# Kernel tuning notes

Hardware: AMD Instinct MI355X
Metric: run time of the kernel (lower is better)

Reference implementation:

```python
import jax, jax.numpy as jnp
import numpy as np

EPS = 1e-5
NEG = -10000.0


def rel_shift(x):
    # x: [B, H, T1, T2] with T2 = 2*T1 - 1 -> returns [B, H, T1, T1]
    B, H, T1, T2 = x.shape
    x = jnp.pad(x, ((0, 0), (0, 0), (0, 0), (1, 0)))        # [B,H,T1,T2+1]
    x = x.reshape(B, H, T2 + 1, T1)[:, :, 1:, :].reshape(B, H, T1, T2)
    return x[:, :, :, : T2 // 2 + 1]


def setup_inputs() -> dict:
    key = jax.random.key(0)
    B, C, T, H = 4, 512, 1024, 8
    ks = jax.random.split(key, 16)
    s = 0.02
    inp = {
        "x": jax.random.normal(ks[0], (B, C, T), jnp.float32),
        "pos_emb": jax.random.normal(ks[1], (1, C, 2 * T - 1), jnp.float32),
        "x_mask": jnp.ones((B, 1, T), jnp.float32),
        "gamma": jnp.ones((C,), jnp.float32),
        "beta": jnp.zeros((C,), jnp.float32),
        "Wq": jax.random.normal(ks[2], (C, C), jnp.float32) * s,
        "bq": jnp.zeros((C,), jnp.float32),
        "Wk": jax.random.normal(ks[3], (C, C), jnp.float32) * s,
        "bk": jnp.zeros((C,), jnp.float32),
        "Wv": jax.random.normal(ks[4], (C, C), jnp.float32) * s,
        "bv": jnp.zeros((C,), jnp.float32),
        "Wp": jax.random.normal(ks[5], (C, C), jnp.float32) * s,
        "u_bias": jax.random.normal(ks[6], (H, C // H), jnp.float32) * s,
        "v_bias": jax.random.normal(ks[7], (H, C // H), jnp.float32) * s,
        "Wo": jax.random.normal(ks[8], (C, C), jnp.float32) * s,
        "bo": jnp.zeros((C,), jnp.float32),
    }
    return inp


def reference(x, pos_emb, x_mask, gamma, beta, Wq, bq, Wk, bk, Wv, bv, Wp,
              u_bias, v_bias, Wo, bo):
    B, C, T = x.shape
    H, Dh = u_bias.shape

    # channel LayerNorm (axis=1)
    mean = jnp.mean(x, axis=1, keepdims=True)
    var = jnp.mean((x - mean) ** 2, axis=1, keepdims=True)
    xn = (x - mean) * jax.lax.rsqrt(var + EPS)
    xn = xn * gamma[None, :, None] + beta[None, :, None]

    conv1x1 = lambda W, b, z: jnp.einsum('oc,bct->bot', W, z) + b[None, :, None]
    q = conv1x1(Wq, bq, xn).reshape(B, H, Dh, T)
    k = conv1x1(Wk, bk, xn).reshape(B, H, Dh, T)
    v = conv1x1(Wv, bv, xn).reshape(B, H, Dh, T)
    p = jnp.einsum('oc,xct->xot', Wp, pos_emb)          # [1, C, 2T-1], no bias
    p = p.reshape(p.shape[0], H, Dh, -1)[0]             # [H, Dh, 2T-1]

    content = jnp.einsum('bhdt,bhds->bhts', q + u_bias[None, :, :, None], k)
    pos = jnp.einsum('bhdt,hds->bhts', q + v_bias[None, :, :, None], p)
    pos = rel_shift(pos)                                 # [B, H, T, T]

    score = (content + pos) / jnp.sqrt(jnp.float32(C))
    attn_mask = x_mask[:, :, None, :] * x_mask[:, :, :, None]  # [B,1,T,T]
    score = jnp.where(attn_mask == 0, NEG, score)
    attn = jax.nn.softmax(score, axis=-1)

    # context[d,t] = sum_s v[d,s] * attn[s,t]
    ctx = jnp.einsum('bhds,bhst->bhdt', v, attn).reshape(B, C, T)
    return jnp.einsum('oc,bct->bot', Wo, ctx) + bo[None, :, None]
```

## Files before the change

kernel.cpp:

```cpp
#include <hip/hip_runtime.h>
#include <hip/hip_bf16.h>

typedef unsigned short u16;
typedef __bf16 bf16_t;
typedef bf16_t bf16x8 __attribute__((ext_vector_type(8)));
typedef float f32x4 __attribute__((ext_vector_type(4)));
typedef u16 u16x8 __attribute__((ext_vector_type(8)));

#define MFMA16(A,B,C) __builtin_amdgcn_mfma_f32_16x16x32_bf16(A,B,C,0,0,0)

#define CB 512
#define TT 1024
#define NH 8
#define DH 64
static __constant__ float kScale = 0.044194173824159216f;

static __device__ __forceinline__ u16 f2b(float f) {
  unsigned u = __float_as_uint(f);
  unsigned r = u + 0x7FFFu + ((u >> 16) & 1u);
  return (u16)(r >> 16);
}
static __device__ __forceinline__ float b2f(u16 u) {
  return __uint_as_float(((unsigned)u) << 16);
}
static __device__ __forceinline__ bf16x8 ldb8(const u16* p) {
  return *reinterpret_cast<const bf16x8*>(p);
}

__global__ __launch_bounds__(256)
void convert5(const float* __restrict__ Wq, const float* __restrict__ Wk,
              const float* __restrict__ Wv, const float* __restrict__ Wp,
              const float* __restrict__ Wo,
              u16* __restrict__ Wstk, u16* __restrict__ WoB)
{
  int i = blockIdx.x * 256 + threadIdx.x;
  int sel = i >> 15, loc = i & 32767;
  const float* src = (sel == 0) ? Wq : (sel == 1) ? Wk : (sel == 2) ? Wv
                   : (sel == 3) ? Wp : Wo;
  const float4 a = ((const float4*)src)[loc * 2 + 0];
  const float4 b = ((const float4*)src)[loc * 2 + 1];
  u16x8 o;
  o[0] = f2b(a.x); o[1] = f2b(a.y); o[2] = f2b(a.z); o[3] = f2b(a.w);
  o[4] = f2b(b.x); o[5] = f2b(b.y); o[6] = f2b(b.z); o[7] = f2b(b.w);
  u16* dst = (sel < 4) ? (Wstk + (size_t)i * 8) : (WoB + (size_t)loc * 8);
  *(u16x8*)dst = o;
}

__global__ __launch_bounds__(256)
void transpose_pe(const float* __restrict__ pe, u16* __restrict__ posT)
{
  __shared__ float tile[64][65];
  int j0 = blockIdx.x * 64, c0 = blockIdx.y * 64;
  for (int e = threadIdx.x; e < 4096; e += 256) {
    int cc = e >> 6, jj = e & 63;
    int j = j0 + jj;
    tile[jj][cc] = (j < 2047) ? pe[(size_t)(c0 + cc) * 2047 + j] : 0.f;
  }
  __syncthreads();
  for (int e = threadIdx.x; e < 4096; e += 256) {
    int jj = e >> 6, cc = e & 63;
    posT[(size_t)(j0 + jj) * 512 + c0 + cc] = f2b(tile[jj][cc]);
  }
}

__global__ __launch_bounds__(256)
void ln_kernel(const float* __restrict__ x, const float* __restrict__ gamma,
               const float* __restrict__ beta, u16* __restrict__ xnT)
{
  __shared__ float sred[8][33], ssred[8][33];
  int tl = threadIdx.x & 31, cg = threadIdx.x >> 5;
  int t = blockIdx.x * 32 + tl;
  int b = blockIdx.y;
  const float* xb = x + (size_t)b * CB * TT + t;
  float s = 0.f, ss = 0.f;
  for (int c = cg * 64; c < cg * 64 + 64; ++c) {
    float v = xb[(size_t)c * TT];
    s += v; ss += v * v;
  }
  sred[cg][tl] = s; ssred[cg][tl] = ss;
  __syncthreads();
  float S = 0.f, SS = 0.f;
  #pragma unroll
  for (int g = 0; g < 8; ++g) { S += sred[g][tl]; SS += ssred[g][tl]; }
  float mean = S * (1.f / 512.f);
  float var = SS * (1.f / 512.f) - mean * mean;
  float rstd = rsqrtf(var + 1e-5f);
  u16* orow = xnT + ((size_t)b * TT + t) * CB;
  for (int c8 = 0; c8 < 8; ++c8) {
    int c = cg * 64 + c8 * 8;
    u16x8 o;
    #pragma unroll
    for (int j = 0; j < 8; ++j) {
      float v = xb[(size_t)(c + j) * TT];
      o[j] = f2b((v - mean) * rstd * gamma[c + j] + beta[c + j]);
    }
    *(u16x8*)(orow + c) = o;
  }
}

template<int K, int OMODE>
__global__ __launch_bounds__(256)
void gemm2(const u16* __restrict__ A, const u16* __restrict__ XT,
           long xStride, long oStride, int Nout,
           const float* __restrict__ b0, void* __restrict__ outv)
{
  const int tid = threadIdx.x, w = tid >> 6, lane = tid & 63;
  const int ln16 = lane & 15, kg = lane >> 4;
  const int wm = w & 1, wn = w >> 1;
  const int m0 = blockIdx.y * 64 + wm * 32;
  const int n0 = blockIdx.x * 128 + wn * 64;
  const int z = blockIdx.z;
  const u16* Ar = A + (size_t)(m0 + ln16) * K + kg * 8;
  const u16* Br = XT + (size_t)z * xStride + (size_t)(n0 + ln16) * K + kg * 8;
  f32x4 acc[2][4] = {};
  #pragma unroll 2
  for (int ks = 0; ks < K / 32; ++ks) {
    bf16x8 a[2], bb[4];
    #pragma unroll
    for (int mt = 0; mt < 2; ++mt) a[mt] = ldb8(Ar + (size_t)mt * 16 * K + ks * 32);
    #pragma unroll
    for (int nt = 0; nt < 4; ++nt) bb[nt] = ldb8(Br + (size_t)nt * 16 * K + ks * 32);
    #pragma unroll
    for (int mt = 0; mt < 2; ++mt)
      #pragma unroll
      for (int nt = 0; nt < 4; ++nt)
        acc[mt][nt] = MFMA16(a[mt], bb[nt], acc[mt][nt]);
  }
  float add[2][4];
  #pragma unroll
  for (int mt = 0; mt < 2; ++mt)
    #pragma unroll
    for (int jr = 0; jr < 4; ++jr)
      add[mt][jr] = b0 ? b0[m0 + mt * 16 + kg * 4 + jr] : 0.f;
  #pragma unroll
  for (int mt = 0; mt < 2; ++mt)
    #pragma unroll
    for (int nt = 0; nt < 4; ++nt) {
      const int n = n0 + nt * 16 + ln16;
      if constexpr (OMODE == 0) {
        float* out = (float*)outv;
        #pragma unroll
        for (int jr = 0; jr < 4; ++jr)
          out[(size_t)z * oStride + (size_t)(m0 + mt * 16 + kg * 4 + jr) * Nout + n] =
              acc[mt][nt][jr] + add[mt][jr];
      } else {
        const int m_low = m0 + mt * 16;
        const size_t o = (size_t)z * oStride +
                         ((size_t)(m_low >> 6) * Nout + n) * 64 + (m_low & 63) + kg * 4;
        ushort4 s4;
        s4.x = f2b(acc[mt][nt][0] + add[mt][0]);
        s4.y = f2b(acc[mt][nt][1] + add[mt][1]);
        s4.z = f2b(acc[mt][nt][2] + add[mt][2]);
        s4.w = f2b(acc[mt][nt][3] + add[mt][3]);
        *reinterpret_cast<ushort4*>((u16*)outv + o) = s4;
      }
    }
}

__global__ __launch_bounds__(256)
void proj_qkv2(const u16* __restrict__ Wstk, const u16* __restrict__ xnT,
               const float* __restrict__ bq, const float* __restrict__ ub,
               const float* __restrict__ bk, const float* __restrict__ bv,
               u16* __restrict__ quB, u16* __restrict__ kB, u16* __restrict__ vB)
{
  const int tid = threadIdx.x, w = tid >> 6, lane = tid & 63;
  const int ln16 = lane & 15, kg = lane >> 4;
  const int wm = w & 1, wn = w >> 1;
  const int my = blockIdx.y;
  const int sec = my >> 3;
  const int m0l = (my & 7) * 64 + wm * 32;
  const int n0 = blockIdx.x * 128 + wn * 64;
  const int z = blockIdx.z;
  const long XS = (long)TT * CB;
  const long QS = (long)NH * TT * DH;
  const u16* Ar = Wstk + (size_t)(sec * 512 + m0l + ln16) * 512 + kg * 8;
  const u16* Br = xnT + (size_t)z * XS + (size_t)(n0 + ln16) * 512 + kg * 8;
  f32x4 acc[2][4] = {};
  #pragma unroll 2
  for (int ks = 0; ks < 16; ++ks) {
    bf16x8 a[2], bb[4];
    #pragma unroll
    for (int mt = 0; mt < 2; ++mt) a[mt] = ldb8(Ar + (size_t)mt * 16 * 512 + ks * 32);
    #pragma unroll
    for (int nt = 0; nt < 4; ++nt) bb[nt] = ldb8(Br + (size_t)nt * 16 * 512 + ks * 32);
    #pragma unroll
    for (int mt = 0; mt < 2; ++mt)
      #pragma unroll
      for (int nt = 0; nt < 4; ++nt)
        acc[mt][nt] = MFMA16(a[mt], bb[nt], acc[mt][nt]);
  }
  float add[2][4];
  #pragma unroll
  for (int mt = 0; mt < 2; ++mt)
    #pragma unroll
    for (int jr = 0; jr < 4; ++jr) {
      int m = m0l + mt * 16 + kg * 4 + jr;
      add[mt][jr] = (sec == 0) ? (bq[m] + ub[m]) : (sec == 1) ? bk[m] : bv[m];
    }
  if (sec < 2) {
    u16* dst = sec ? kB : quB;
    #pragma unroll
    for (int mt = 0; mt < 2; ++mt)
      #pragma unroll
      for (int nt = 0; nt < 4; ++nt) {
        const int n = n0 + nt * 16 + ln16;
        const int m_low = m0l + mt * 16;
        const size_t o = (size_t)z * QS +
                         ((size_t)(m_low >> 6) * TT + n) * 64 + (m_low & 63) + kg * 4;
        ushort4 s4;
        s4.x = f2b(acc[mt][nt][0] + add[mt][0]);
        s4.y = f2b(acc[mt][nt][1] + add[mt][1]);
        s4.z = f2b(acc[mt][nt][2] + add[mt][2]);
        s4.w = f2b(acc[mt][nt][3] + add[mt][3]);
        *reinterpret_cast<ushort4*>(dst + o) = s4;
      }
  } else {
    #pragma unroll
    for (int mt = 0; mt < 2; ++mt)
      #pragma unroll
      for (int nt = 0; nt < 4; ++nt) {
        const int n = n0 + nt * 16 + ln16;
        #pragma unroll
        for (int jr = 0; jr < 4; ++jr)
          vB[(size_t)z * QS + (size_t)(m0l + mt * 16 + kg * 4 + jr) * TT + n] =
              f2b(acc[mt][nt][jr] + add[mt][jr]);
      }
  }
}

__global__ __launch_bounds__(256)
void corr_kernel(const u16* __restrict__ pp, const float* __restrict__ ub,
                 const float* __restrict__ vb, float* __restrict__ corr)
{
  const int h = blockIdx.y;
  const int j = blockIdx.x * 256 + threadIdx.x;
  __shared__ float dl[64];
  if (threadIdx.x < 64)
    dl[threadIdx.x] = vb[h * 64 + threadIdx.x] - ub[h * 64 + threadIdx.x];
  __syncthreads();
  const u16* prow = pp + ((size_t)h * 2048 + j) * 64;
  float s = 0.f;
  #pragma unroll
  for (int d8 = 0; d8 < 8; ++d8) {
    union { bf16x8 v; u16 u[8]; } pu;
    pu.v = ldb8(prow + d8 * 8);
    #pragma unroll
    for (int e = 0; e < 8; ++e) s += b2f(pu.u[e]) * dl[d8 * 8 + e];
  }
  corr[h * 2048 + j] = s;
}

__global__ __launch_bounds__(256)
void stats_mfma(const u16* __restrict__ qu, const u16* __restrict__ kk_,
                const u16* __restrict__ pp, const float* __restrict__ corr,
                const float* __restrict__ xmask, float* __restrict__ ls)
{
  const int tid = threadIdx.x;
  const int w = tid >> 6, lane = tid & 63;
  const int ln16 = lane & 15, kg = lane >> 4;
  const int bid = blockIdx.x;
  const int bh = (bid & 7) + 8 * ((bid >> 3) & 3);
  const int rest = bid >> 5;
  const int qi0 = (rest & 31) * 32;
  const int part = rest >> 5;
  const int b = bh >> 3, h = bh & 7;
  const u16* quP = qu + (size_t)bh * TT * DH;
  const u16* kP  = kk_ + (size_t)bh * TT * DH;
  const u16* pP  = pp + (size_t)h * 2048 * DH;
  const float* corrP = corr + (h << 11);

  __shared__ u16 G[4][32][100];
  __shared__ float red[4][32];

  bf16x8 qa[2][2];
  #pragma unroll
  for (int mt = 0; mt < 2; ++mt)
    #pragma unroll
    for (int kc = 0; kc < 2; ++kc)
      qa[mt][kc] = ldb8(&quP[(size_t)(qi0 + mt * 16 + ln16) * DH + kc * 32 + kg * 8]);
  float aq[2][4];
  #pragma unroll
  for (int mt = 0; mt < 2; ++mt)
    #pragma unroll
    for (int jr = 0; jr < 4; ++jr)
      aq[mt][jr] = (xmask[b * TT + qi0 + mt * 16 + kg * 4 + jr] - 1.f) * 10000.f;

  float rs[2][4] = {};
  for (int c = 0; c < 2; ++c) {
    const int ki0 = (part * 8 + c * 4 + w) * 64;
    const int j0 = ki0 - qi0 + 992;
    #pragma unroll
    for (int nt = 0; nt < 6; ++nt) {
      const size_t po = (size_t)(j0 + nt * 16 + ln16) * DH + kg * 8;
      bf16x8 pb0 = ldb8(&pP[po]);
      bf16x8 pb1 = ldb8(&pP[po + 32]);
      const float cval = corrP[j0 + nt * 16 + ln16];
      #pragma unroll
      for (int mt = 0; mt < 2; ++mt) {
        f32x4 g = {0.f, 0.f, 0.f, 0.f};
        g = MFMA16(qa[mt][0], pb0, g);
        g = MFMA16(qa[mt][1], pb1, g);
        #pragma unroll
        for (int jr = 0; jr < 4; ++jr)
          G[w][mt * 16 + kg * 4 + jr][nt * 16 + ln16] = f2b(g[jr] + cval);
      }
    }
    #pragma unroll
    for (int nt = 0; nt < 4; ++nt) {
      const size_t ko = (size_t)(ki0 + nt * 16 + ln16) * DH + kg * 8;
      bf16x8 kb0 = ldb8(&kP[ko]);
      bf16x8 kb1 = ldb8(&kP[ko + 32]);
      const float ak = (xmask[b * TT + ki0 + nt * 16 + ln16] - 1.f) * 10000.f;
      #pragma unroll
      for (int mt = 0; mt < 2; ++mt) {
        f32x4 dd = {0.f, 0.f, 0.f, 0.f};
        dd = MFMA16(qa[mt][0], kb0, dd);
        dd = MFMA16(qa[mt][1], kb1, dd);
        #pragma unroll
        for (int jr = 0; jr < 4; ++jr) {
          const int qrow = mt * 16 + kg * 4 + jr;
          const int u = nt * 16 + ln16 - qrow + 31;
          const float s = (dd[jr] + b2f(G[w][qrow][u])) * kScale + aq[mt][jr] + ak;
          rs[mt][jr] += __expf(s);
        }
      }
    }
  }
  #pragma unroll
  for (int mt = 0; mt < 2; ++mt)
    #pragma unroll
    for (int jr = 0; jr < 4; ++jr) {
      float v = rs[mt][jr];
      v += __shfl_xor(v, 1); v += __shfl_xor(v, 2);
      v += __shfl_xor(v, 4); v += __shfl_xor(v, 8);
      rs[mt][jr] = v;
    }
  if (ln16 == 0) {
    #pragma unroll
    for (int mt = 0; mt < 2; ++mt)
      #pragma unroll
      for (int jr = 0; jr < 4; ++jr)
        red[w][mt * 16 + kg * 4 + jr] = rs[mt][jr];
  }
  __syncthreads();
  if (tid < 32)
    ls[(size_t)part * 32768 + (size_t)bh * TT + qi0 + tid] =
        red[0][tid] + red[1][tid] + red[2][tid] + red[3][tid];
}

__global__ __launch_bounds__(256)
void ctx_mfma(const u16* __restrict__ qu, const u16* __restrict__ kk_,
              const u16* __restrict__ vv, const u16* __restrict__ pp,
              const float* __restrict__ corr, const float* __restrict__ xmask,
              const float* __restrict__ ls, u16* __restrict__ ctx2)
{
  const int tid = threadIdx.x;
  const int w = tid >> 6, lane = tid & 63;
  const int ln16 = lane & 15, kg = lane >> 4;
  const int bid = blockIdx.x;
  const int bh = (bid & 7) + 8 * ((bid >> 3) & 3);
  const int rest = bid >> 5;
  const int t0 = (rest & 15) * 64;
  const int part = rest >> 4;
  const int b = bh >> 3, h = bh & 7;
  const u16* quP = qu + (size_t)bh * TT * DH;
  const u16* kP  = kk_ + (size_t)bh * TT * DH;
  const u16* vP  = vv + (size_t)bh * DH * TT;
  const u16* pP  = pp + (size_t)h * 2048 * DH;
  const float* corrP = corr + (h << 11);
  const float* lsP = ls + (size_t)bh * TT;

  __shared__ u16 G[4][16][84];
  __shared__ __align__(16) u16 P[64][80];

  bf16x8 ka[4][2];
  #pragma unroll
  for (int nt = 0; nt < 4; ++nt)
    #pragma unroll
    for (int kc = 0; kc < 2; ++kc)
      ka[nt][kc] = ldb8(&kP[(size_t)(t0 + nt * 16 + ln16) * DH + kc * 32 + kg * 8]);
  float at4[4];
  #pragma unroll
  for (int nt = 0; nt < 4; ++nt)
    at4[nt] = (xmask[b * TT + t0 + nt * 16 + ln16] - 1.f) * 10000.f;

  f32x4 cacc[4] = {};
  for (int qc = part * 4; qc < part * 4 + 4; ++qc) {
    const int qw = qc * 64 + w * 16;
    const int j0 = t0 - qw + 1008;
    const size_t qo = (size_t)(qw + ln16) * DH + kg * 8;
    bf16x8 qa0 = ldb8(&quP[qo]), qa1 = ldb8(&quP[qo + 32]);
    #pragma unroll
    for (int nt = 0; nt < 5; ++nt) {
      const size_t po = (size_t)(j0 + nt * 16 + ln16) * DH + kg * 8;
      bf16x8 pb0 = ldb8(&pP[po]), pb1 = ldb8(&pP[po + 32]);
      const float cval = corrP[j0 + nt * 16 + ln16];
      f32x4 g = {0.f, 0.f, 0.f, 0.f};
      g = MFMA16(qa0, pb0, g);
      g = MFMA16(qa1, pb1, g);
      #pragma unroll
      for (int jr = 0; jr < 4; ++jr)
        G[w][kg * 4 + jr][nt * 16 + ln16] = f2b(g[jr] + cval);
    }
    float linv[4], aqv[4];
    #pragma unroll
    for (int jr = 0; jr < 4; ++jr) {
      const int qi = qw + kg * 4 + jr;
      linv[jr] = 1.f / (lsP[qi] + lsP[32768 + qi]);
      aqv[jr] = (xmask[b * TT + qi] - 1.f) * 10000.f;
    }
    __syncthreads();
    #pragma unroll
    for (int nt = 0; nt < 4; ++nt) {
      f32x4 dd = {0.f, 0.f, 0.f, 0.f};
      dd = MFMA16(qa0, ka[nt][0], dd);
      dd = MFMA16(qa1, ka[nt][1], dd);
      unsigned lo = 0, hi = 0;
      #pragma unroll
      for (int jr = 0; jr < 4; ++jr) {
        const int qrow = kg * 4 + jr;
        const int u = nt * 16 + ln16 - qrow + 15;
        const float s = (dd[jr] + b2f(G[w][qrow][u])) * kScale + aqv[jr] + at4[nt];
        const float e = __expf(s) * linv[jr];
        const unsigned bb = f2b(e);
        if (jr == 0) lo = bb; else if (jr == 1) lo |= bb << 16;
        else if (jr == 2) hi = bb; else hi |= bb << 16;
      }
      *reinterpret_cast<uint2*>(&P[nt * 16 + ln16][w * 16 + kg * 4]) = make_uint2(lo, hi);
    }
    __syncthreads();
    const size_t vbase = (size_t)(w * 16 + ln16) * TT + qc * 64 + kg * 8;
    bf16x8 vf0 = ldb8(&vP[vbase]), vf1 = ldb8(&vP[vbase + 32]);
    #pragma unroll
    for (int nt = 0; nt < 4; ++nt) {
      bf16x8 pb0 = *reinterpret_cast<const bf16x8*>(&P[nt * 16 + ln16][kg * 8]);
      bf16x8 pb1 = *reinterpret_cast<const bf16x8*>(&P[nt * 16 + ln16][32 + kg * 8]);
      cacc[nt] = MFMA16(vf0, pb0, cacc[nt]);
      cacc[nt] = MFMA16(vf1, pb1, cacc[nt]);
    }
  }
  #pragma unroll
  for (int nt = 0; nt < 4; ++nt) {
    const int t = t0 + nt * 16 + ln16;
    ushort4 s4;
    s4.x = f2b(cacc[nt][0]); s4.y = f2b(cacc[nt][1]);
    s4.z = f2b(cacc[nt][2]); s4.w = f2b(cacc[nt][3]);
    *reinterpret_cast<ushort4*>(
      &ctx2[((size_t)b * TT + t) * 2048 + part * 512 + h * 64 + w * 16 + kg * 4]) = s4;
  }
}

__global__ __launch_bounds__(256)
void reduce_ctx(const u16* __restrict__ ctx2, u16* __restrict__ ctxS)
{
  int i = blockIdx.x * 256 + threadIdx.x;
  int row = i >> 6;
  int c0 = (i & 63) * 8;
  const u16* src = ctx2 + (size_t)row * 2048 + c0;
  float s[8] = {};
  #pragma unroll
  for (int p = 0; p < 4; ++p) {
    union { u16x8 v; u16 u[8]; } t;
    t.v = *(const u16x8*)(src + p * 512);
    #pragma unroll
    for (int e = 0; e < 8; ++e) s[e] += b2f(t.u[e]);
  }
  u16x8 o;
  #pragma unroll
  for (int e = 0; e < 8; ++e) o[e] = f2b(s[e]);
  *(u16x8*)(ctxS + (size_t)row * 512 + c0) = o;
}

extern "C" void kernel_launch(void* const* d_in, const int* in_sizes, int n_in,
                              void* d_out, int out_size, void* d_ws, size_t ws_size,
                              hipStream_t stream)
{
  (void)in_sizes; (void)n_in; (void)out_size;
  const float* x     = (const float*)d_in[0];
  const float* pe    = (const float*)d_in[1];
  const float* xm    = (const float*)d_in[2];
  const float* gamma = (const float*)d_in[3];
  const float* beta  = (const float*)d_in[4];
  const float* Wq    = (const float*)d_in[5];
  const float* bq    = (const float*)d_in[6];
  const float* Wk    = (const float*)d_in[7];
  const float* bk    = (const float*)d_in[8];
  const float* Wv    = (const float*)d_in[9];
  const float* bv    = (const float*)d_in[10];
  const float* Wp    = (const float*)d_in[11];
  const float* ub    = (const float*)d_in[12];
  const float* vb    = (const float*)d_in[13];
  const float* Wo    = (const float*)d_in[14];
  const float* bo    = (const float*)d_in[15];

  char* ws = (char*)d_ws;
  u16*  quB  = (u16*) (ws + 0);
  u16*  ctxS = (u16*) (ws + 0);
  u16*  kB   = (u16*) (ws + 4194304);
  u16*  vB   = (u16*) (ws + 8388608);
  u16*  pB   = (u16*) (ws + 12582912);
  float* corrB = (float*)(ws + 14680064);
  float* lsB = (float*)(ws + 14745600);
  u16*  WoB  = (u16*) (ws + 15007744);
  u16*  ctx2 = (u16*) (ws + 15532032);
  u16*  xnT  = (u16*) (ws + 15532032);
  u16*  posT = (u16*) (ws + 19726336);
  u16*  Wstk = (u16*) (ws + 21823488);
  if (ws_size < 32309248) return;

  dim3 blk(256);

  convert5<<<dim3(640), blk, 0, stream>>>(Wq, Wk, Wv, Wp, Wo, Wstk, WoB);
  transpose_pe<<<dim3(32, 8), blk, 0, stream>>>(pe, posT);
  ln_kernel<<<dim3(32, 4), blk, 0, stream>>>(x, gamma, beta, xnT);

  proj_qkv2<<<dim3(8, 24, 4), blk, 0, stream>>>(Wstk, xnT, bq, ub, bk, bv, quB, kB, vB);
  gemm2<512, 1><<<dim3(16, 8, 1), blk, 0, stream>>>(
      Wstk + (size_t)1536 * 512, posT, 0, 0, 2048, nullptr, pB);
  corr_kernel<<<dim3(8, 8), blk, 0, stream>>>(pB, ub, vb, corrB);

  stats_mfma<<<dim3(2048), blk, 0, stream>>>(quB, kB, pB, corrB, xm, lsB);
  ctx_mfma<<<dim3(2048), blk, 0, stream>>>(quB, kB, vB, pB, corrB, xm, lsB, ctx2);
  reduce_ctx<<<dim3(1024), blk, 0, stream>>>(ctx2, ctxS);

  gemm2<512, 0><<<dim3(8, 8, 4), blk, 0, stream>>>(
      WoB, ctxS, (long)TT * CB, (long)CB * TT, TT, bo, (float*)d_out);
}
```

Measured before the change: 207.8 us.

## Fold softmax scale into q, use exp2, move normalization onto V

The softmax scale and log2(e) are folded into the stored q+u projection and the correction term, so the score loops call exp2f directly. The mask bias is preloaded into the MFMA accumulator instead of being added per element. Row normalization by the softmax sum moves out of ctx_mfma into a new vscale kernel that scales V by 1/l, which removes per-tile reciprocal loads from the attention loop. The P LDS padding shrinks. The cost is an extra kernel launch and a pass over V, plus a small change in bf16 rounding because q is scaled before quantization.

```diff
diff --git a/kernel.cpp b/kernel.cpp
--- a/kernel.cpp
+++ b/kernel.cpp
@@ -1,5 +1,6 @@
 #include <hip/hip_runtime.h>
 #include <hip/hip_bf16.h>
+#include <cmath>
 
 typedef unsigned short u16;
 typedef __bf16 bf16_t;
@@ -13,7 +14,8 @@
 #define TT 1024
 #define NH 8
 #define DH 64
-static __constant__ float kScale = 0.044194173824159216f;
+#define ALPHA (0.044194173824159216f * 1.4426950408889634f)
+#define MASKL 14426.950408889634f
 
 static __device__ __forceinline__ u16 f2b(float f) {
   unsigned u = __float_as_uint(f);
@@ -189,6 +191,7 @@
       for (int nt = 0; nt < 4; ++nt)
         acc[mt][nt] = MFMA16(a[mt], bb[nt], acc[mt][nt]);
   }
+  const float scl = (sec == 0) ? ALPHA : 1.f;
   float add[2][4];
   #pragma unroll
   for (int mt = 0; mt < 2; ++mt)
@@ -208,10 +211,10 @@
         const size_t o = (size_t)z * QS +
                          ((size_t)(m_low >> 6) * TT + n) * 64 + (m_low & 63) + kg * 4;
         ushort4 s4;
-        s4.x = f2b(acc[mt][nt][0] + add[mt][0]);
-        s4.y = f2b(acc[mt][nt][1] + add[mt][1]);
-        s4.z = f2b(acc[mt][nt][2] + add[mt][2]);
-        s4.w = f2b(acc[mt][nt][3] + add[mt][3]);
+        s4.x = f2b((acc[mt][nt][0] + add[mt][0]) * scl);
+        s4.y = f2b((acc[mt][nt][1] + add[mt][1]) * scl);
+        s4.z = f2b((acc[mt][nt][2] + add[mt][2]) * scl);
+        s4.w = f2b((acc[mt][nt][3] + add[mt][3]) * scl);
         *reinterpret_cast<ushort4*>(dst + o) = s4;
       }
   } else {
@@ -247,7 +250,7 @@
     #pragma unroll
     for (int e = 0; e < 8; ++e) s += b2f(pu.u[e]) * dl[d8 * 8 + e];
   }
-  corr[h * 2048 + j] = s;
+  corr[h * 2048 + j] = s * ALPHA;
 }
 
 __global__ __launch_bounds__(256)
@@ -283,7 +286,7 @@
   for (int mt = 0; mt < 2; ++mt)
     #pragma unroll
     for (int jr = 0; jr < 4; ++jr)
-      aq[mt][jr] = (xmask[b * TT + qi0 + mt * 16 + kg * 4 + jr] - 1.f) * 10000.f;
+      aq[mt][jr] = (xmask[b * TT + qi0 + mt * 16 + kg * 4 + jr] - 1.f) * MASKL;
 
   float rs[2][4] = {};
   for (int c = 0; c < 2; ++c) {
@@ -310,18 +313,17 @@
       const size_t ko = (size_t)(ki0 + nt * 16 + ln16) * DH + kg * 8;
       bf16x8 kb0 = ldb8(&kP[ko]);
       bf16x8 kb1 = ldb8(&kP[ko + 32]);
-      const float ak = (xmask[b * TT + ki0 + nt * 16 + ln16] - 1.f) * 10000.f;
+      const float ak = (xmask[b * TT + ki0 + nt * 16 + ln16] - 1.f) * MASKL;
       #pragma unroll
       for (int mt = 0; mt < 2; ++mt) {
-        f32x4 dd = {0.f, 0.f, 0.f, 0.f};
+        f32x4 dd = { aq[mt][0] + ak, aq[mt][1] + ak, aq[mt][2] + ak, aq[mt][3] + ak };
         dd = MFMA16(qa[mt][0], kb0, dd);
         dd = MFMA16(qa[mt][1], kb1, dd);
         #pragma unroll
         for (int jr = 0; jr < 4; ++jr) {
           const int qrow = mt * 16 + kg * 4 + jr;
           const int u = nt * 16 + ln16 - qrow + 31;
-          const float s = (dd[jr] + b2f(G[w][qrow][u])) * kScale + aq[mt][jr] + ak;
-          rs[mt][jr] += __expf(s);
+          rs[mt][jr] += exp2f(dd[jr] + b2f(G[w][qrow][u]));
         }
       }
     }
@@ -349,10 +351,31 @@
 }
 
 __global__ __launch_bounds__(256)
+void vscale(u16* __restrict__ vv, const float* __restrict__ ls)
+{
+  int i = blockIdx.x * 256 + threadIdx.x;
+  int bh = i >> 13;
+  int rem = i & 8191;
+  int d = rem >> 7;
+  int qi0 = (rem & 127) * 8;
+  const float* lsP = ls + bh * 1024 + qi0;
+  u16* row = vv + ((size_t)bh * 64 + d) * 1024 + qi0;
+  union { u16x8 v; u16 u[8]; } t;
+  t.v = *(u16x8*)row;
+  u16x8 o;
+  #pragma unroll
+  for (int e = 0; e < 8; ++e) {
+    float linv = __builtin_amdgcn_rcpf(lsP[e] + lsP[32768 + e]);
+    o[e] = f2b(b2f(t.u[e]) * linv);
+  }
+  *(u16x8*)row = o;
+}
+
+__global__ __launch_bounds__(256)
 void ctx_mfma(const u16* __restrict__ qu, const u16* __restrict__ kk_,
               const u16* __restrict__ vv, const u16* __restrict__ pp,
               const float* __restrict__ corr, const float* __restrict__ xmask,
-              const float* __restrict__ ls, u16* __restrict__ ctx2)
+              u16* __restrict__ ctx2)
 {
   const int tid = threadIdx.x;
   const int w = tid >> 6, lane = tid & 63;
@@ -368,10 +391,9 @@
   const u16* vP  = vv + (size_t)bh * DH * TT;
   const u16* pP  = pp + (size_t)h * 2048 * DH;
   const float* corrP = corr + (h << 11);
-  const float* lsP = ls + (size_t)bh * TT;
 
   __shared__ u16 G[4][16][84];
-  __shared__ __align__(16) u16 P[64][80];
+  __shared__ __align__(16) u16 P[64][72];
 
   bf16x8 ka[4][2];
   #pragma unroll
@@ -382,7 +404,7 @@
   float at4[4];
   #pragma unroll
   for (int nt = 0; nt < 4; ++nt)
-    at4[nt] = (xmask[b * TT + t0 + nt * 16 + ln16] - 1.f) * 10000.f;
+    at4[nt] = (xmask[b * TT + t0 + nt * 16 + ln16] - 1.f) * MASKL;
 
   f32x4 cacc[4] = {};
   for (int qc = part * 4; qc < part * 4 + 4; ++qc) {
@@ -402,17 +424,15 @@
       for (int jr = 0; jr < 4; ++jr)
         G[w][kg * 4 + jr][nt * 16 + ln16] = f2b(g[jr] + cval);
     }
-    float linv[4], aqv[4];
-    #pragma unroll
-    for (int jr = 0; jr < 4; ++jr) {
-      const int qi = qw + kg * 4 + jr;
-      linv[jr] = 1.f / (lsP[qi] + lsP[32768 + qi]);
-      aqv[jr] = (xmask[b * TT + qi] - 1.f) * 10000.f;
-    }
+    float aqv[4];
+    #pragma unroll
+    for (int jr = 0; jr < 4; ++jr)
+      aqv[jr] = (xmask[b * TT + qw + kg * 4 + jr] - 1.f) * MASKL;
     __syncthreads();
     #pragma unroll
     for (int nt = 0; nt < 4; ++nt) {
-      f32x4 dd = {0.f, 0.f, 0.f, 0.f};
+      f32x4 dd = { aqv[0] + at4[nt], aqv[1] + at4[nt],
+                   aqv[2] + at4[nt], aqv[3] + at4[nt] };
       dd = MFMA16(qa0, ka[nt][0], dd);
       dd = MFMA16(qa1, ka[nt][1], dd);
       unsigned lo = 0, hi = 0;
@@ -420,8 +440,7 @@
       for (int jr = 0; jr < 4; ++jr) {
         const int qrow = kg * 4 + jr;
         const int u = nt * 16 + ln16 - qrow + 15;
-        const float s = (dd[jr] + b2f(G[w][qrow][u])) * kScale + aqv[jr] + at4[nt];
-        const float e = __expf(s) * linv[jr];
+        const float e = exp2f(dd[jr] + b2f(G[w][qrow][u]));
         const unsigned bb = f2b(e);
         if (jr == 0) lo = bb; else if (jr == 1) lo |= bb << 16;
         else if (jr == 2) hi = bb; else hi |= bb << 16;
@@ -520,7 +539,8 @@
   corr_kernel<<<dim3(8, 8), blk, 0, stream>>>(pB, ub, vb, corrB);
 
   stats_mfma<<<dim3(2048), blk, 0, stream>>>(quB, kB, pB, corrB, xm, lsB);
-  ctx_mfma<<<dim3(2048), blk, 0, stream>>>(quB, kB, vB, pB, corrB, xm, lsB, ctx2);
+  vscale<<<dim3(1024), blk, 0, stream>>>(vB, lsB);
+  ctx_mfma<<<dim3(2048), blk, 0, stream>>>(quB, kB, vB, pB, corrB, xm, ctx2);
   reduce_ctx<<<dim3(1024), blk, 0, stream>>>(ctx2, ctxS);
 
   gemm2<512, 0><<<dim3(8, 8, 4), blk, 0, stream>>>(
```

New measurement: 210.9 us. No clear change (+1.5%).
